# Kernel optimization log

Hardware: AMD Instinct MI355X
Metric: run time of the kernel (lower is better)

## Reference

```python
import jax, jax.numpy as jnp
import numpy as np

B, C, W, H, N = 8, 128, 48, 48, 8192


def setup_inputs() -> dict:
    key = jax.random.key(0)
    ks = jax.random.split(key, 16)
    s = 1.0 / np.sqrt(C)
    inp = {
        "feat0": jax.random.normal(ks[0], (B, C, W, H), jnp.float32),
        "feat1": jax.random.normal(ks[1], (B, C, N), jnp.float32),
        "geo_embed": jax.random.normal(ks[2], (B, W * H, C), jnp.float32),
        # Linear weights stored as [in, out]; biases [out].
        "Wq": jax.random.normal(ks[3], (C, C), jnp.float32) * s,
        "bq": jnp.zeros((C,), jnp.float32),
        "Wk": jax.random.normal(ks[4], (C, C), jnp.float32) * s,
        "bk": jnp.zeros((C,), jnp.float32),
        "Wv": jax.random.normal(ks[5], (C, C), jnp.float32) * s,
        "bv": jnp.zeros((C,), jnp.float32),
        "Wo": jax.random.normal(ks[6], (C, C), jnp.float32) * s,
        "bo": jnp.zeros((C,), jnp.float32),
        "Wg": jax.random.normal(ks[7], (C, C), jnp.float32) * s,
        "bg": jnp.zeros((C,), jnp.float32),
        "Wgate": jax.random.normal(ks[8], (2 * C, 1), jnp.float32) * (1.0 / np.sqrt(2 * C)),
        "bgate": jnp.zeros((1,), jnp.float32),
    }
    return inp


def reference(feat0, feat1, geo_embed, Wq, bq, Wk, bk, Wv, bv, Wo, bo, Wg, bg, Wgate, bgate):
    b, c, w, h = feat0.shape
    # b c w h -> b (w h) c
    q_in = feat0.reshape(b, c, w * h).transpose(0, 2, 1)
    pq = q_in @ Wq + bq  # [b, wh, c]

    geo = geo_embed @ Wg + bg  # [b, wh, c]
    gate = jax.nn.sigmoid(jnp.concatenate([pq, geo], axis=-1) @ Wgate + bgate)  # [b, wh, 1]
    pq = pq + gate * geo

    kv_in = feat1.transpose(0, 2, 1)  # [b, n, c]
    pk = kv_in @ Wk + bk
    pv = kv_in @ Wv + bv

    energy = jnp.einsum('bqc,bnc->bqn', pq, pk)  # [b, wh, n]
    # NOTE: original scales AFTER softmax (non-standard, faithful):
    attention = jax.nn.softmax(energy, axis=-1) / jnp.sqrt(jnp.asarray(c, energy.dtype))
    out = jnp.einsum('bqn,bnc->bqc', attention, pv) @ Wo + bo  # [b, wh, c]
    out = out.transpose(0, 2, 1).reshape(b, c, w, h)

    geo_r = geo.transpose(0, 2, 1).reshape(b, c, w, h)
    out = out * (1.0 + jax.nn.sigmoid(geo_r))
    out = out + feat0
    return out
```

## Files before the change

### kernel.cpp

```cpp
#include <hip/hip_runtime.h>

#define B_ 8
#define C_ 128
#define WH_ 2304
#define N_ 8192

typedef unsigned short u16;
typedef float f32x4 __attribute__((ext_vector_type(4)));
typedef short s16x8 __attribute__((ext_vector_type(8)));
typedef short s16x4 __attribute__((ext_vector_type(4)));
typedef unsigned int u32x2 __attribute__((ext_vector_type(2)));

typedef const unsigned int __attribute__((address_space(1))) ga_u32;
typedef unsigned int __attribute__((address_space(3))) lds_u32;

#define LOG2E 1.4426950408889634f
#define MOFF  64.0f

#define MFMA16K16(a,b,c) __builtin_amdgcn_mfma_f32_16x16x16bf16_1k(a,b,c,0,0,0)

__device__ __forceinline__ float bf2f(u16 u){
    union { unsigned int i; float f; } x; x.i = ((unsigned int)u) << 16; return x.f;
}
__device__ __forceinline__ u16 f2bf(float f){
    union { float f; unsigned int i; } x; x.f = f;
    unsigned int r = x.i + 0x7fffu + ((x.i >> 16) & 1u);
    return (u16)(r >> 16);
}
__device__ __forceinline__ int swz(int row, int col){
    return row*128 + ((((col >> 3) ^ (row & 15)) << 3) | (col & 7));
}
__device__ __forceinline__ f32x4 fzero(){ f32x4 z = {0.f, 0.f, 0.f, 0.f}; return z; }
__device__ __forceinline__ f32x4 mfma16(s16x8 a, s16x8 b, f32x4 c){
    return __builtin_amdgcn_mfma_f32_16x16x32_bf16(a, b, c, 0, 0, 0);
}
__device__ __forceinline__ void gld16(const void* g, void* l){
    __builtin_amdgcn_global_load_lds((ga_u32*)g, (lds_u32*)l, 16, 0, 0);
}
__device__ __forceinline__ s16x8 ldsf(const u16* p){ return *(const s16x8*)p; }
__device__ __forceinline__ s16x4 ldsf4(const u16* p){ return *(const s16x4*)p; }
__device__ __forceinline__ s16x8 cvt8(const float* p){
    s16x8 r;
    #pragma unroll
    for (int j = 0; j < 8; j++) r[j] = (short)f2bf(p[j]);
    return r;
}

__global__ __launch_bounds__(256) void k_prep(
    const float* __restrict__ Wq, const float* __restrict__ Wk,
    const float* __restrict__ Wv, const float* __restrict__ Wo,
    const float* __restrict__ Wg, u16* __restrict__ Wt)
{
    const int gid = blockIdx.x*256 + threadIdx.x;
    const int mi = gid >> 14, e = gid & 16383;
    const int o = e >> 7, i = e & 127;
    const float* src = (mi==0)?Wq:(mi==1)?Wk:(mi==2)?Wv:(mi==3)?Wo:Wg;
    Wt[mi*16384 + o*128 + i] = f2bf(src[i*128 + o]);
}

__device__ __forceinline__ void proj_kv_body(
    char* smem, int blk,
    const float* __restrict__ feat1,
    const float* __restrict__ bk, const float* __restrict__ bv,
    const u16* __restrict__ Wt,
    u16* __restrict__ Kb, u16* __restrict__ Vb)
{
    u16* Wks = (u16*)smem;
    u16* Wvs = (u16*)(smem + 32768);
    u16* Af  = (u16*)(smem + 65536);
    const int t = threadIdx.x;
    const int b = blk >> 5;
    const int n0 = (blk & 31) * 256;
    for (int idx = t; idx < 2048; idx += 256){
        int o = idx >> 4, i0 = (idx & 15) << 3;
        *(s16x8*)&Wks[o*128 + (((i0 >> 3) ^ (o & 15)) << 3)] = *(const s16x8*)&Wt[16384 + o*128 + i0];
        *(s16x8*)&Wvs[o*128 + (((i0 >> 3) ^ (o & 15)) << 3)] = *(const s16x8*)&Wt[32768 + o*128 + i0];
    }
    for (int idx = t; idx < 256*128; idx += 256){
        int nl = idx & 255, c = idx >> 8;
        Af[swz(nl, c)] = f2bf(feat1[((size_t)b*C_ + c)*N_ + n0 + nl]);
    }
    __syncthreads();
    const int lane = t & 63, w = t >> 6, qq = lane >> 4, m = lane & 15;
    s16x8 aA[4][4];
    #pragma unroll
    for (int rt = 0; rt < 4; rt++){
        const int ar = w*64 + rt*16 + m;
        #pragma unroll
        for (int kt = 0; kt < 4; kt++)
            aA[rt][kt] = ldsf(&Af[ar*128 + (((kt*4 + qq) ^ (ar & 15)) << 3)]);
    }
    f32x4 acc[4][8];
    #pragma unroll
    for (int rt = 0; rt < 4; rt++){
        #pragma unroll
        for (int ct = 0; ct < 8; ct++) acc[rt][ct] = fzero();
    }
    #pragma unroll
    for (int kt = 0; kt < 4; kt++){
        #pragma unroll
        for (int ct = 0; ct < 8; ct++){
            const int bn = ct*16 + m;
            const s16x8 bf = ldsf(&Wks[bn*128 + (((kt*4 + qq) ^ (bn & 15)) << 3)]);
            #pragma unroll
            for (int rt = 0; rt < 4; rt++) acc[rt][ct] = mfma16(aA[rt][kt], bf, acc[rt][ct]);
        }
    }
    __syncthreads();
    u16* Ko = (u16*)(smem + 65536);
    #pragma unroll
    for (int ct = 0; ct < 8; ct++){
        const int col = ct*16 + m;
        const float bkv = bk[col];
        #pragma unroll
        for (int rt = 0; rt < 4; rt++){
            #pragma unroll
            for (int i = 0; i < 4; i++)
                Ko[swz(w*64 + rt*16 + qq*4 + i, col)] = f2bf(acc[rt][ct][i] + bkv);
        }
    }
    #pragma unroll
    for (int j = 0; j < 16; j++){
        const int chunk = j*64 + lane;
        const int row = w*64 + (chunk >> 4);
        const int cb = chunk & 15;
        s16x8 v = ldsf(&Ko[row*128 + ((cb ^ (row & 15)) << 3)]);
        *(s16x8*)&Kb[((size_t)b*N_ + n0 + row)*C_ + cb*8] = v;
    }
    #pragma unroll
    for (int rt = 0; rt < 4; rt++){
        #pragma unroll
        for (int ct = 0; ct < 8; ct++) acc[rt][ct] = fzero();
    }
    #pragma unroll
    for (int kt = 0; kt < 4; kt++){
        #pragma unroll
        for (int ct = 0; ct < 8; ct++){
            const int bn = ct*16 + m;
            const s16x8 bf = ldsf(&Wvs[bn*128 + (((kt*4 + qq) ^ (bn & 15)) << 3)]);
            #pragma unroll
            for (int rt = 0; rt < 4; rt++) acc[rt][ct] = mfma16(aA[rt][kt], bf, acc[rt][ct]);
        }
    }
    __syncthreads();
    u16* Tv = (u16*)(smem + 65536);
    #pragma unroll
    for (int ct = 0; ct < 8; ct++){
        const int col = ct*16 + m;
        const float bvv = bv[col];
        #pragma unroll
        for (int rt = 0; rt < 4; rt++){
            #pragma unroll
            for (int i = 0; i < 4; i++)
                Tv[col*258 + w*64 + rt*16 + qq*4 + i] = f2bf(acc[rt][ct][i] + bvv);
        }
    }
    __syncthreads();
    for (int idx = t; idx < 128*256; idx += 256){
        int c = idx >> 8, nl = idx & 255;
        Vb[((size_t)b*C_ + c)*N_ + n0 + nl] = Tv[c*258 + nl];
    }
}

__device__ __forceinline__ void proj_qg_body(
    char* smem, int blk,
    const float* __restrict__ feat0, const float* __restrict__ geo,
    const float* __restrict__ bq, const float* __restrict__ bg,
    const float* __restrict__ Wgate, const float* __restrict__ bgate,
    const u16* __restrict__ Wt,
    u16* __restrict__ Qb, u16* __restrict__ Gb)
{
    u16* Wqs = (u16*)smem;
    u16* Wgs = (u16*)(smem + 32768);
    u16* Aq  = (u16*)(smem + 65536);
    const int t = threadIdx.x;
    const int b = blk / 18;
    const int r0 = (blk % 18) * 128;
    for (int idx = t; idx < 2048; idx += 256){
        int o = idx >> 4, i0 = (idx & 15) << 3;
        *(s16x8*)&Wqs[o*128 + (((i0 >> 3) ^ (o & 15)) << 3)] = *(const s16x8*)&Wt[o*128 + i0];
        *(s16x8*)&Wgs[o*128 + (((i0 >> 3) ^ (o & 15)) << 3)] = *(const s16x8*)&Wt[65536 + o*128 + i0];
    }
    for (int idx = t; idx < 128*128; idx += 256){
        int r = idx & 127, c = idx >> 7;
        Aq[swz(r, c)] = f2bf(feat0[((size_t)b*C_ + c)*WH_ + r0 + r]);
    }
    __syncthreads();
    const int lane = t & 63, w = t >> 6, qq = lane >> 4, m = lane & 15;
    s16x8 aQ[2][4], aG[2][4];
    #pragma unroll
    for (int rt = 0; rt < 2; rt++){
        const int ar = w*32 + rt*16 + m;
        #pragma unroll
        for (int kt = 0; kt < 4; kt++){
            aQ[rt][kt] = ldsf(&Aq[ar*128 + (((kt*4 + qq) ^ (ar & 15)) << 3)]);
            aG[rt][kt] = cvt8(&geo[((size_t)b*WH_ + r0 + ar)*C_ + kt*32 + qq*8]);
        }
    }
    f32x4 accq[2][8], accg[2][8];
    #pragma unroll
    for (int rt = 0; rt < 2; rt++){
        #pragma unroll
        for (int ct = 0; ct < 8; ct++){ accq[rt][ct] = fzero(); accg[rt][ct] = fzero(); }
    }
    #pragma unroll
    for (int kt = 0; kt < 4; kt++){
        #pragma unroll
        for (int ct = 0; ct < 8; ct++){
            const int bn = ct*16 + m;
            const s16x8 b1 = ldsf(&Wqs[bn*128 + (((kt*4 + qq) ^ (bn & 15)) << 3)]);
            const s16x8 b2 = ldsf(&Wgs[bn*128 + (((kt*4 + qq) ^ (bn & 15)) << 3)]);
            #pragma unroll
            for (int rt = 0; rt < 2; rt++){
                accq[rt][ct] = mfma16(aQ[rt][kt], b1, accq[rt][ct]);
                accg[rt][ct] = mfma16(aG[rt][kt], b2, accg[rt][ct]);
            }
        }
    }
    float bqv[8], bgv[8], w1v[8], w2v[8];
    #pragma unroll
    for (int ct = 0; ct < 8; ct++){
        int col = ct*16 + m;
        bqv[ct] = bq[col]; bgv[ct] = bg[col];
        w1v[ct] = Wgate[col]; w2v[ct] = Wgate[C_ + col];
    }
    const float bg0 = bgate[0];
    float gate[2][4];
    #pragma unroll
    for (int rt = 0; rt < 2; rt++){
        #pragma unroll
        for (int i = 0; i < 4; i++){
            float p = 0.f;
            #pragma unroll
            for (int ct = 0; ct < 8; ct++)
                p += (accq[rt][ct][i] + bqv[ct]) * w1v[ct] + (accg[rt][ct][i] + bgv[ct]) * w2v[ct];
            #pragma unroll
            for (int off = 1; off < 16; off <<= 1) p += __shfl_xor(p, off, 64);
            gate[rt][i] = 1.f / (1.f + __expf(-(p + bg0)));
        }
    }
    __syncthreads();
    u16* St = Aq;
    #pragma unroll
    for (int ct = 0; ct < 8; ct++){
        #pragma unroll
        for (int rt = 0; rt < 2; rt++){
            #pragma unroll
            for (int i = 0; i < 4; i++){
                const float ge = accg[rt][ct][i] + bgv[ct];
                const float pq = accq[rt][ct][i] + bqv[ct] + gate[rt][i] * ge;
                St[swz(w*32 + rt*16 + qq*4 + i, ct*16 + m)] = f2bf(pq * LOG2E);
            }
        }
    }
    #pragma unroll
    for (int j = 0; j < 8; j++){
        const int chunk = j*64 + lane;
        const int row = w*32 + (chunk >> 4);
        const int cb = chunk & 15;
        s16x8 v = ldsf(&St[row*128 + ((cb ^ (row & 15)) << 3)]);
        *(s16x8*)&Qb[((size_t)b*WH_ + r0 + row)*C_ + cb*8] = v;
    }
    #pragma unroll
    for (int ct = 0; ct < 8; ct++){
        #pragma unroll
        for (int rt = 0; rt < 2; rt++){
            #pragma unroll
            for (int i = 0; i < 4; i++)
                St[swz(w*32 + rt*16 + qq*4 + i, ct*16 + m)] = f2bf(accg[rt][ct][i] + bgv[ct]);
        }
    }
    #pragma unroll
    for (int j = 0; j < 8; j++){
        const int chunk = j*64 + lane;
        const int row = w*32 + (chunk >> 4);
        const int cb = chunk & 15;
        s16x8 v = ldsf(&St[row*128 + ((cb ^ (row & 15)) << 3)]);
        *(s16x8*)&Gb[((size_t)b*WH_ + r0 + row)*C_ + cb*8] = v;
    }
}

__global__ __launch_bounds__(256) void k_proj(
    const float* __restrict__ feat1,
    const float* __restrict__ bk, const float* __restrict__ bv,
    const float* __restrict__ feat0, const float* __restrict__ geo,
    const float* __restrict__ bq, const float* __restrict__ bg,
    const float* __restrict__ Wgate, const float* __restrict__ bgate,
    const u16* __restrict__ Wt,
    u16* __restrict__ Kb, u16* __restrict__ Vb,
    u16* __restrict__ Qb, u16* __restrict__ Gb)
{
    __shared__ __attribute__((aligned(16))) char smem[65536 + 66048];
    if (blockIdx.x < 256)
        proj_kv_body(smem, blockIdx.x, feat1, bk, bv, Wt, Kb, Vb);
    else
        proj_qg_body(smem, blockIdx.x - 256, feat0, geo, bq, bg, Wgate, bgate, Wt, Qb, Gb);
}

__global__ __launch_bounds__(1024, 4) void k_flash(
    const u16* __restrict__ Qb, const u16* __restrict__ Kb, const u16* __restrict__ Vb,
    u16* __restrict__ Opart, float* __restrict__ Lp)
{
    __shared__ __attribute__((aligned(16))) u16 KP0[128*128];
    __shared__ __attribute__((aligned(16))) u16 KP1[128*128];
    __shared__ __attribute__((aligned(16))) u16 Vt0[128*128];
    __shared__ __attribute__((aligned(16))) u16 Vt1[128*128];
    const int t = threadIdx.x;
    const int lane = t & 63, w = t >> 6;
    const int q = lane >> 4, m = lane & 15;
    const int b = blockIdx.x & 7;
    const int s = blockIdx.x >> 3;

    f32x4 o[8];
    float lr;
    s16x8 qf[4];

    auto issue = [&](int k){
        const int u = s*18 + k;
        const int n0 = (u & 63) * 128;
        u16* KPd = (k & 1) ? KP1 : KP0;
        u16* Vtd = (k & 1) ? Vt1 : Vt0;
        #pragma unroll
        for (int j = 0; j < 2; j++){
            const int r = w*8 + j*4 + q;
            gld16(Kb + ((size_t)b*N_ + n0 + r)*C_ + ((m ^ (r & 15)) << 3), &KPd[(w*8 + j*4)*128]);
            gld16(Vb + ((size_t)b*C_ + r)*N_ + n0 + ((m ^ (r & 15)) << 3), &Vtd[(w*8 + j*4)*128]);
        }
    };
    auto load_q = [&](int qb){
        const size_t qrow0 = (size_t)b*WH_ + qb*256;
        #pragma unroll
        for (int kt = 0; kt < 4; kt++)
            qf[kt] = *(const s16x8*)&Qb[(qrow0 + w*16 + m)*C_ + kt*32 + q*8];
    };
    auto zero_acc = [&](){
        #pragma unroll
        for (int ct = 0; ct < 8; ct++) o[ct] = fzero();
        lr = 0.f;
    };
    auto flush = [&](int qb){
        const int sf = (qb * 64) / 18;
        const size_t pbase = ((size_t)(b*9 + qb)*5 + (s - sf)) * 256;
        #pragma unroll
        for (int ct = 0; ct < 8; ct++){
            u32x2 pk;
            pk.x = (unsigned int)f2bf(o[ct][0]) | ((unsigned int)f2bf(o[ct][1]) << 16);
            pk.y = (unsigned int)f2bf(o[ct][2]) | ((unsigned int)f2bf(o[ct][3]) << 16);
            *(u32x2*)&Opart[(pbase + w*16 + m)*128 + ct*16 + q*4] = pk;
        }
        float l0 = lr;
        l0 += __shfl_xor(l0, 16, 64); l0 += __shfl_xor(l0, 32, 64);
        if (q == 0) Lp[pbase + w*16 + m] = l0;
    };

    issue(0);
    int cur_qb = (s*18) >> 6;
    load_q(cur_qb);
    zero_acc();

    for (int k = 0; k < 18; k++){
        __syncthreads();
        if (k < 17) issue(k + 1);
        const u16* KPc = (k & 1) ? KP1 : KP0;
        const u16* Vtc = (k & 1) ? Vt1 : Vt0;

        #pragma unroll
        for (int h = 0; h < 2; h++){
            s16x4 pexp[4];
            #pragma unroll
            for (int n2 = 0; n2 < 4; n2++){
                const int nt = h*4 + n2;
                f32x4 s0 = fzero();
                const int bn = nt*16 + m;
                #pragma unroll
                for (int kt = 0; kt < 4; kt++){
                    s16x8 kf = ldsf(&KPc[bn*128 + (((kt*4 + q) ^ (bn & 15)) << 3)]);
                    s0 = mfma16(kf, qf[kt], s0);
                }
                #pragma unroll
                for (int i = 0; i < 4; i++){
                    float e0 = exp2f(s0[i] - MOFF);
                    lr += e0;
                    pexp[n2][i] = (short)f2bf(e0);
                }
            }
            #pragma unroll
            for (int ct = 0; ct < 8; ct++){
                const int cc = ct*16 + m;
                #pragma unroll
                for (int n2 = 0; n2 < 4; n2++){
                    const int g = h*4 + n2;
                    s16x4 vf = ldsf4(&Vtc[cc*128 + ((((g*2 + (q >> 1)) ^ (cc & 15)) << 3) | ((q & 1) * 4))]);
                    o[ct] = MFMA16K16(vf, pexp[n2], o[ct]);
                }
            }
        }
        const int nqb = (k < 17) ? ((s*18 + k + 1) >> 6) : -1;
        if (nqb != cur_qb){
            flush(cur_qb);
            if (nqb >= 0){ load_q(nqb); zero_acc(); cur_qb = nqb; }
        }
    }
}

__global__ __launch_bounds__(256) void k_out(
    const u16* __restrict__ Opart, const float* __restrict__ Lp,
    const float* __restrict__ bo, const u16* __restrict__ Wt,
    const u16* __restrict__ Gb, const float* __restrict__ feat0,
    float* __restrict__ outp)
{
    __shared__ __attribute__((aligned(16))) u16 AO[128*128];
    __shared__ u16 Tr[128*130];
    const int t = threadIdx.x;
    const int bqt = blockIdx.x;
    const int qt2 = bqt >> 1, half = bqt & 1;
    const int b = qt2 / 9, qb = qt2 % 9;
    const int gr0 = qb*256 + half*128;
    const u16* WoT = Wt + 49152;
    const float rsC = 0.088388347648318447f;
    const int sf = (qb*64) / 18;
    const int sl = (qb*64 + 63) / 18;
    const int cnt = sl - sf + 1;
    for (int idx = t; idx < 128*16; idx += 256){
        int r = idx >> 4, cb = idx & 15;
        float num[8];
        #pragma unroll
        for (int j = 0; j < 8; j++) num[j] = 0.f;
        float den = 0.f;
        for (int ss = 0; ss < cnt; ss++){
            const size_t base = ((size_t)qt2*5 + ss)*256 + half*128 + r;
            s16x8 v = *(const s16x8*)&Opart[base*128 + cb*8];
            #pragma unroll
            for (int j = 0; j < 8; j++) num[j] += bf2f((u16)v[j]);
            den += Lp[base];
        }
        const float sc = rsC / den;
        s16x8 o8;
        #pragma unroll
        for (int j = 0; j < 8; j++) o8[j] = (short)f2bf(num[j] * sc);
        *(s16x8*)&AO[r*128 + ((cb ^ (r & 15)) << 3)] = o8;
    }
    __syncthreads();
    const int lane = t & 63, w = t >> 6;
    const int q = lane >> 4, m = lane & 15;
    const int rw = w * 32;
    f32x4 acc[2][8];
    #pragma unroll
    for (int rt = 0; rt < 2; rt++){
        #pragma unroll
        for (int ct = 0; ct < 8; ct++) acc[rt][ct] = fzero();
    }
    #pragma unroll
    for (int kt = 0; kt < 4; kt++){
        s16x8 a0, a1;
        { const int ar = rw + m;      a0 = ldsf(&AO[ar*128 + (((kt*4 + q) ^ (ar & 15)) << 3)]); }
        { const int ar = rw + 16 + m; a1 = ldsf(&AO[ar*128 + (((kt*4 + q) ^ (ar & 15)) << 3)]); }
        #pragma unroll
        for (int ct = 0; ct < 8; ct++){
            const s16x8 bb = *(const s16x8*)&WoT[(ct*16 + m)*128 + kt*32 + q*8];
            acc[0][ct] = mfma16(a0, bb, acc[0][ct]);
            acc[1][ct] = mfma16(a1, bb, acc[1][ct]);
        }
    }
    #pragma unroll
    for (int ct = 0; ct < 8; ct++){
        const int col = ct*16 + m;
        const float bov = bo[col];
        #pragma unroll
        for (int rt = 0; rt < 2; rt++){
            #pragma unroll
            for (int i = 0; i < 4; i++){
                const int rl = rw + rt*16 + q*4 + i;
                const float gv = bf2f(Gb[((size_t)b*WH_ + gr0 + rl)*C_ + col]);
                const float sg = 1.f / (1.f + __expf(-gv));
                Tr[rl*130 + col] = f2bf((acc[rt][ct][i] + bov) * (1.f + sg));
            }
        }
    }
    __syncthreads();
    for (int idx = t; idx < 128*128; idx += 256){
        int c = idx >> 7, wh = idx & 127;
        float v = bf2f(Tr[wh*130 + c]) + feat0[(size_t)(b*C_ + c)*WH_ + gr0 + wh];
        outp[(size_t)(b*C_ + c)*WH_ + gr0 + wh] = v;
    }
}

extern "C" void kernel_launch(void* const* d_in, const int* in_sizes, int n_in,
                              void* d_out, int out_size, void* d_ws, size_t ws_size,
                              hipStream_t stream)
{
    (void)in_sizes; (void)n_in; (void)out_size; (void)ws_size;
    const float* feat0 = (const float*)d_in[0];
    const float* feat1 = (const float*)d_in[1];
    const float* geo   = (const float*)d_in[2];
    const float* Wq = (const float*)d_in[3];  const float* bq = (const float*)d_in[4];
    const float* Wk = (const float*)d_in[5];  const float* bk = (const float*)d_in[6];
    const float* Wv = (const float*)d_in[7];  const float* bv = (const float*)d_in[8];
    const float* Wo = (const float*)d_in[9];  const float* bo = (const float*)d_in[10];
    const float* Wg = (const float*)d_in[11]; const float* bg = (const float*)d_in[12];
    const float* Wgate = (const float*)d_in[13]; const float* bgate = (const float*)d_in[14];
    float* outp = (float*)d_out;
    char* ws = (char*)d_ws;
    size_t off = 0;
    auto alloc = [&](size_t bytes) -> void* {
        void* p = (void*)(ws + off);
        off += (bytes + 255) & ~(size_t)255;
        return p;
    };
    u16* Qb = (u16*)alloc((size_t)B_*WH_*C_*2);
    u16* Gb = (u16*)alloc((size_t)B_*WH_*C_*2);
    u16* Kb = (u16*)alloc((size_t)B_*N_*C_*2);
    u16* Vb = (u16*)alloc((size_t)B_*N_*C_*2);
    u16* Opart = (u16*)alloc((size_t)72*5*256*128*2);
    float* Lp  = (float*)alloc((size_t)72*5*256*4);
    u16* Wt = (u16*)alloc((size_t)5*16384*2);

    k_prep <<<dim3(320), dim3(256), 0, stream>>>(Wq, Wk, Wv, Wo, Wg, Wt);
    k_proj <<<dim3(400), dim3(256), 0, stream>>>(feat1, bk, bv, feat0, geo, bq, bg,
                                                 Wgate, bgate, Wt, Kb, Vb, Qb, Gb);
    k_flash<<<dim3(256), dim3(1024), 0, stream>>>(Qb, Kb, Vb, Opart, Lp);
    k_out  <<<dim3(144), dim3(256), 0, stream>>>(Opart, Lp, bo, Wt, Gb, feat0, outp);
}
```

Baseline: 297.6 us.

## Use K=32 MFMA for PV via key permutation and slim projection kernel

The flash kernel permutes key rows during the LDS load so that two 16x16x16 MFMAs per V-tile can be merged into one 16x16x32 bf16 MFMA. The -MOFF softmax offset moves into the MFMA accumulator init, which removes one subtract per score. The projection kernel now runs 512 threads per block with half the rows per wave and reads weights straight from global memory instead of staging them in LDS. Input loads are vectorized, which cuts shared memory use and aims to raise occupancy. The trade-off is more global/L2 weight traffic and a permutation that must exactly match the P-fragment layout.

```diff
diff --git a/kernel.cpp b/kernel.cpp
--- a/kernel.cpp
+++ b/kernel.cpp
@@ -17,8 +17,6 @@
 #define LOG2E 1.4426950408889634f
 #define MOFF  64.0f
 
-#define MFMA16K16(a,b,c) __builtin_amdgcn_mfma_f32_16x16x16bf16_1k(a,b,c,0,0,0)
-
 __device__ __forceinline__ float bf2f(u16 u){
     union { unsigned int i; float f; } x; x.i = ((unsigned int)u) << 16; return x.f;
 }
@@ -31,6 +29,7 @@
     return row*128 + ((((col >> 3) ^ (row & 15)) << 3) | (col & 7));
 }
 __device__ __forceinline__ f32x4 fzero(){ f32x4 z = {0.f, 0.f, 0.f, 0.f}; return z; }
+__device__ __forceinline__ f32x4 fmoff(){ f32x4 z = {-MOFF, -MOFF, -MOFF, -MOFF}; return z; }
 __device__ __forceinline__ f32x4 mfma16(s16x8 a, s16x8 b, f32x4 c){
     return __builtin_amdgcn_mfma_f32_16x16x32_bf16(a, b, c, 0, 0, 0);
 }
@@ -38,7 +37,6 @@
     __builtin_amdgcn_global_load_lds((ga_u32*)g, (lds_u32*)l, 16, 0, 0);
 }
 __device__ __forceinline__ s16x8 ldsf(const u16* p){ return *(const s16x8*)p; }
-__device__ __forceinline__ s16x4 ldsf4(const u16* p){ return *(const s16x4*)p; }
 __device__ __forceinline__ s16x8 cvt8(const float* p){
     s16x8 r;
     #pragma unroll
@@ -65,34 +63,31 @@
     const u16* __restrict__ Wt,
     u16* __restrict__ Kb, u16* __restrict__ Vb)
 {
-    u16* Wks = (u16*)smem;
-    u16* Wvs = (u16*)(smem + 32768);
-    u16* Af  = (u16*)(smem + 65536);
+    u16* Af = (u16*)smem;
     const int t = threadIdx.x;
     const int b = blk >> 5;
     const int n0 = (blk & 31) * 256;
-    for (int idx = t; idx < 2048; idx += 256){
-        int o = idx >> 4, i0 = (idx & 15) << 3;
-        *(s16x8*)&Wks[o*128 + (((i0 >> 3) ^ (o & 15)) << 3)] = *(const s16x8*)&Wt[16384 + o*128 + i0];
-        *(s16x8*)&Wvs[o*128 + (((i0 >> 3) ^ (o & 15)) << 3)] = *(const s16x8*)&Wt[32768 + o*128 + i0];
-    }
-    for (int idx = t; idx < 256*128; idx += 256){
-        int nl = idx & 255, c = idx >> 8;
-        Af[swz(nl, c)] = f2bf(feat1[((size_t)b*C_ + c)*N_ + n0 + nl]);
+    for (int idx = t; idx < 8192; idx += 512){
+        const int nl = (idx & 63) << 2, c = idx >> 6;
+        const f32x4 v = *(const f32x4*)&feat1[((size_t)b*C_ + c)*N_ + n0 + nl];
+        Af[swz(nl+0, c)] = f2bf(v[0]); Af[swz(nl+1, c)] = f2bf(v[1]);
+        Af[swz(nl+2, c)] = f2bf(v[2]); Af[swz(nl+3, c)] = f2bf(v[3]);
     }
     __syncthreads();
     const int lane = t & 63, w = t >> 6, qq = lane >> 4, m = lane & 15;
-    s16x8 aA[4][4];
-    #pragma unroll
-    for (int rt = 0; rt < 4; rt++){
-        const int ar = w*64 + rt*16 + m;
+    s16x8 aA[2][4];
+    #pragma unroll
+    for (int rt = 0; rt < 2; rt++){
+        const int ar = w*32 + rt*16 + m;
         #pragma unroll
         for (int kt = 0; kt < 4; kt++)
             aA[rt][kt] = ldsf(&Af[ar*128 + (((kt*4 + qq) ^ (ar & 15)) << 3)]);
     }
-    f32x4 acc[4][8];
-    #pragma unroll
-    for (int rt = 0; rt < 4; rt++){
+    const u16* WkT = Wt + 16384;
+    const u16* WvT = Wt + 32768;
+    f32x4 acc[2][8];
+    #pragma unroll
+    for (int rt = 0; rt < 2; rt++){
         #pragma unroll
         for (int ct = 0; ct < 8; ct++) acc[rt][ct] = fzero();
     }
@@ -101,34 +96,33 @@
         #pragma unroll
         for (int ct = 0; ct < 8; ct++){
             const int bn = ct*16 + m;
-            const s16x8 bf = ldsf(&Wks[bn*128 + (((kt*4 + qq) ^ (bn & 15)) << 3)]);
-            #pragma unroll
-            for (int rt = 0; rt < 4; rt++) acc[rt][ct] = mfma16(aA[rt][kt], bf, acc[rt][ct]);
-        }
-    }
-    __syncthreads();
-    u16* Ko = (u16*)(smem + 65536);
+            const s16x8 bf = *(const s16x8*)&WkT[bn*128 + kt*32 + qq*8];
+            acc[0][ct] = mfma16(aA[0][kt], bf, acc[0][ct]);
+            acc[1][ct] = mfma16(aA[1][kt], bf, acc[1][ct]);
+        }
+    }
+    u16* Ko = (u16*)smem;
     #pragma unroll
     for (int ct = 0; ct < 8; ct++){
         const int col = ct*16 + m;
         const float bkv = bk[col];
         #pragma unroll
-        for (int rt = 0; rt < 4; rt++){
+        for (int rt = 0; rt < 2; rt++){
             #pragma unroll
             for (int i = 0; i < 4; i++)
-                Ko[swz(w*64 + rt*16 + qq*4 + i, col)] = f2bf(acc[rt][ct][i] + bkv);
-        }
-    }
-    #pragma unroll
-    for (int j = 0; j < 16; j++){
+                Ko[swz(w*32 + rt*16 + qq*4 + i, col)] = f2bf(acc[rt][ct][i] + bkv);
+        }
+    }
+    #pragma unroll
+    for (int j = 0; j < 8; j++){
         const int chunk = j*64 + lane;
-        const int row = w*64 + (chunk >> 4);
+        const int row = w*32 + (chunk >> 4);
         const int cb = chunk & 15;
         s16x8 v = ldsf(&Ko[row*128 + ((cb ^ (row & 15)) << 3)]);
         *(s16x8*)&Kb[((size_t)b*N_ + n0 + row)*C_ + cb*8] = v;
     }
     #pragma unroll
-    for (int rt = 0; rt < 4; rt++){
+    for (int rt = 0; rt < 2; rt++){
         #pragma unroll
         for (int ct = 0; ct < 8; ct++) acc[rt][ct] = fzero();
     }
@@ -137,28 +131,29 @@
         #pragma unroll
         for (int ct = 0; ct < 8; ct++){
             const int bn = ct*16 + m;
-            const s16x8 bf = ldsf(&Wvs[bn*128 + (((kt*4 + qq) ^ (bn & 15)) << 3)]);
-            #pragma unroll
-            for (int rt = 0; rt < 4; rt++) acc[rt][ct] = mfma16(aA[rt][kt], bf, acc[rt][ct]);
-        }
-    }
-    __syncthreads();
-    u16* Tv = (u16*)(smem + 65536);
+            const s16x8 bf = *(const s16x8*)&WvT[bn*128 + kt*32 + qq*8];
+            acc[0][ct] = mfma16(aA[0][kt], bf, acc[0][ct]);
+            acc[1][ct] = mfma16(aA[1][kt], bf, acc[1][ct]);
+        }
+    }
+    __syncthreads();
+    u16* Tv = (u16*)smem;
     #pragma unroll
     for (int ct = 0; ct < 8; ct++){
         const int col = ct*16 + m;
         const float bvv = bv[col];
         #pragma unroll
-        for (int rt = 0; rt < 4; rt++){
+        for (int rt = 0; rt < 2; rt++){
             #pragma unroll
             for (int i = 0; i < 4; i++)
-                Tv[col*258 + w*64 + rt*16 + qq*4 + i] = f2bf(acc[rt][ct][i] + bvv);
-        }
-    }
-    __syncthreads();
-    for (int idx = t; idx < 128*256; idx += 256){
-        int c = idx >> 8, nl = idx & 255;
-        Vb[((size_t)b*C_ + c)*N_ + n0 + nl] = Tv[c*258 + nl];
+                Tv[col*258 + w*32 + rt*16 + qq*4 + i] = f2bf(acc[rt][ct][i] + bvv);
+        }
+    }
+    __syncthreads();
+    for (int idx = t; idx < 16384; idx += 512){
+        const int c = idx >> 7, nl = (idx & 127) << 1;
+        const unsigned int v = *(const unsigned int*)&Tv[c*258 + nl];
+        *(unsigned int*)&Vb[((size_t)b*C_ + c)*N_ + n0 + nl] = v;
     }
 }
 
@@ -170,51 +165,37 @@
     const u16* __restrict__ Wt,
     u16* __restrict__ Qb, u16* __restrict__ Gb)
 {
-    u16* Wqs = (u16*)smem;
-    u16* Wgs = (u16*)(smem + 32768);
-    u16* Aq  = (u16*)(smem + 65536);
+    u16* Aq = (u16*)smem;
     const int t = threadIdx.x;
     const int b = blk / 18;
     const int r0 = (blk % 18) * 128;
-    for (int idx = t; idx < 2048; idx += 256){
-        int o = idx >> 4, i0 = (idx & 15) << 3;
-        *(s16x8*)&Wqs[o*128 + (((i0 >> 3) ^ (o & 15)) << 3)] = *(const s16x8*)&Wt[o*128 + i0];
-        *(s16x8*)&Wgs[o*128 + (((i0 >> 3) ^ (o & 15)) << 3)] = *(const s16x8*)&Wt[65536 + o*128 + i0];
-    }
-    for (int idx = t; idx < 128*128; idx += 256){
-        int r = idx & 127, c = idx >> 7;
-        Aq[swz(r, c)] = f2bf(feat0[((size_t)b*C_ + c)*WH_ + r0 + r]);
+    for (int idx = t; idx < 4096; idx += 512){
+        const int r = (idx & 31) << 2, c = idx >> 5;
+        const f32x4 v = *(const f32x4*)&feat0[((size_t)b*C_ + c)*WH_ + r0 + r];
+        Aq[swz(r+0, c)] = f2bf(v[0]); Aq[swz(r+1, c)] = f2bf(v[1]);
+        Aq[swz(r+2, c)] = f2bf(v[2]); Aq[swz(r+3, c)] = f2bf(v[3]);
     }
     __syncthreads();
     const int lane = t & 63, w = t >> 6, qq = lane >> 4, m = lane & 15;
-    s16x8 aQ[2][4], aG[2][4];
-    #pragma unroll
-    for (int rt = 0; rt < 2; rt++){
-        const int ar = w*32 + rt*16 + m;
-        #pragma unroll
-        for (int kt = 0; kt < 4; kt++){
-            aQ[rt][kt] = ldsf(&Aq[ar*128 + (((kt*4 + qq) ^ (ar & 15)) << 3)]);
-            aG[rt][kt] = cvt8(&geo[((size_t)b*WH_ + r0 + ar)*C_ + kt*32 + qq*8]);
-        }
-    }
-    f32x4 accq[2][8], accg[2][8];
-    #pragma unroll
-    for (int rt = 0; rt < 2; rt++){
-        #pragma unroll
-        for (int ct = 0; ct < 8; ct++){ accq[rt][ct] = fzero(); accg[rt][ct] = fzero(); }
-    }
+    const int ar = w*16 + m;
+    s16x8 aQ[4], aG[4];
+    #pragma unroll
+    for (int kt = 0; kt < 4; kt++){
+        aQ[kt] = ldsf(&Aq[ar*128 + (((kt*4 + qq) ^ (ar & 15)) << 3)]);
+        aG[kt] = cvt8(&geo[((size_t)b*WH_ + r0 + ar)*C_ + kt*32 + qq*8]);
+    }
+    f32x4 accq[8], accg[8];
+    #pragma unroll
+    for (int ct = 0; ct < 8; ct++){ accq[ct] = fzero(); accg[ct] = fzero(); }
     #pragma unroll
     for (int kt = 0; kt < 4; kt++){
         #pragma unroll
         for (int ct = 0; ct < 8; ct++){
             const int bn = ct*16 + m;
-            const s16x8 b1 = ldsf(&Wqs[bn*128 + (((kt*4 + qq) ^ (bn & 15)) << 3)]);
-            const s16x8 b2 = ldsf(&Wgs[bn*128 + (((kt*4 + qq) ^ (bn & 15)) << 3)]);
-            #pragma unroll
-            for (int rt = 0; rt < 2; rt++){
-                accq[rt][ct] = mfma16(aQ[rt][kt], b1, accq[rt][ct]);
-                accg[rt][ct] = mfma16(aG[rt][kt], b2, accg[rt][ct]);
-            }
+            const s16x8 b1 = *(const s16x8*)&Wt[bn*128 + kt*32 + qq*8];
+            const s16x8 b2 = *(const s16x8*)&Wt[65536 + bn*128 + kt*32 + qq*8];
+            accq[ct] = mfma16(aQ[kt], b1, accq[ct]);
+            accg[ct] = mfma16(aG[kt], b2, accg[ct]);
         }
     }
     float bqv[8], bgv[8], w1v[8], w2v[8];
@@ -225,38 +206,31 @@
         w1v[ct] = Wgate[col]; w2v[ct] = Wgate[C_ + col];
     }
     const float bg0 = bgate[0];
-    float gate[2][4];
-    #pragma unroll
-    for (int rt = 0; rt < 2; rt++){
+    float gate[4];
+    #pragma unroll
+    for (int i = 0; i < 4; i++){
+        float p = 0.f;
+        #pragma unroll
+        for (int ct = 0; ct < 8; ct++)
+            p += (accq[ct][i] + bqv[ct]) * w1v[ct] + (accg[ct][i] + bgv[ct]) * w2v[ct];
+        #pragma unroll
+        for (int off = 1; off < 16; off <<= 1) p += __shfl_xor(p, off, 64);
+        gate[i] = 1.f / (1.f + __expf(-(p + bg0)));
+    }
+    u16* St = Aq;
+    #pragma unroll
+    for (int ct = 0; ct < 8; ct++){
         #pragma unroll
         for (int i = 0; i < 4; i++){
-            float p = 0.f;
-            #pragma unroll
-            for (int ct = 0; ct < 8; ct++)
-                p += (accq[rt][ct][i] + bqv[ct]) * w1v[ct] + (accg[rt][ct][i] + bgv[ct]) * w2v[ct];
-            #pragma unroll
-            for (int off = 1; off < 16; off <<= 1) p += __shfl_xor(p, off, 64);
-            gate[rt][i] = 1.f / (1.f + __expf(-(p + bg0)));
-        }
-    }
-    __syncthreads();
-    u16* St = Aq;
-    #pragma unroll
-    for (int ct = 0; ct < 8; ct++){
-        #pragma unroll
-        for (int rt = 0; rt < 2; rt++){
-            #pragma unroll
-            for (int i = 0; i < 4; i++){
-                const float ge = accg[rt][ct][i] + bgv[ct];
-                const float pq = accq[rt][ct][i] + bqv[ct] + gate[rt][i] * ge;
-                St[swz(w*32 + rt*16 + qq*4 + i, ct*16 + m)] = f2bf(pq * LOG2E);
-            }
-        }
-    }
-    #pragma unroll
-    for (int j = 0; j < 8; j++){
+            const float ge = accg[ct][i] + bgv[ct];
+            const float pq = accq[ct][i] + bqv[ct] + gate[i] * ge;
+            St[swz(w*16 + qq*4 + i, ct*16 + m)] = f2bf(pq * LOG2E);
+        }
+    }
+    #pragma unroll
+    for (int j = 0; j < 4; j++){
         const int chunk = j*64 + lane;
-        const int row = w*32 + (chunk >> 4);
+        const int row = w*16 + (chunk >> 4);
         const int cb = chunk & 15;
         s16x8 v = ldsf(&St[row*128 + ((cb ^ (row & 15)) << 3)]);
         *(s16x8*)&Qb[((size_t)b*WH_ + r0 + row)*C_ + cb*8] = v;
@@ -264,23 +238,20 @@
     #pragma unroll
     for (int ct = 0; ct < 8; ct++){
         #pragma unroll
-        for (int rt = 0; rt < 2; rt++){
-            #pragma unroll
-            for (int i = 0; i < 4; i++)
-                St[swz(w*32 + rt*16 + qq*4 + i, ct*16 + m)] = f2bf(accg[rt][ct][i] + bgv[ct]);
-        }
-    }
-    #pragma unroll
-    for (int j = 0; j < 8; j++){
+        for (int i = 0; i < 4; i++)
+            St[swz(w*16 + qq*4 + i, ct*16 + m)] = f2bf(accg[ct][i] + bgv[ct]);
+    }
+    #pragma unroll
+    for (int j = 0; j < 4; j++){
         const int chunk = j*64 + lane;
-        const int row = w*32 + (chunk >> 4);
+        const int row = w*16 + (chunk >> 4);
         const int cb = chunk & 15;
         s16x8 v = ldsf(&St[row*128 + ((cb ^ (row & 15)) << 3)]);
         *(s16x8*)&Gb[((size_t)b*WH_ + r0 + row)*C_ + cb*8] = v;
     }
 }
 
-__global__ __launch_bounds__(256) void k_proj(
+__global__ __launch_bounds__(512, 4) void k_proj(
     const float* __restrict__ feat1,
     const float* __restrict__ bk, const float* __restrict__ bv,
     const float* __restrict__ feat0, const float* __restrict__ geo,
@@ -290,7 +261,7 @@
     u16* __restrict__ Kb, u16* __restrict__ Vb,
     u16* __restrict__ Qb, u16* __restrict__ Gb)
 {
-    __shared__ __attribute__((aligned(16))) char smem[65536 + 66048];
+    __shared__ __attribute__((aligned(16))) char smem[66048];
     if (blockIdx.x < 256)
         proj_kv_body(smem, blockIdx.x, feat1, bk, bv, Wt, Kb, Vb);
     else
@@ -323,7 +294,8 @@
         #pragma unroll
         for (int j = 0; j < 2; j++){
             const int r = w*8 + j*4 + q;
-            gld16(Kb + ((size_t)b*N_ + n0 + r)*C_ + ((m ^ (r & 15)) << 3), &KPd[(w*8 + j*4)*128]);
+            const int pr = (r & 96) | ((r & 12) << 1) | ((r & 16) >> 2) | (r & 3);
+            gld16(Kb + ((size_t)b*N_ + n0 + pr)*C_ + ((m ^ (r & 15)) << 3), &KPd[(w*8 + j*4)*128]);
             gld16(Vb + ((size_t)b*C_ + r)*N_ + n0 + ((m ^ (r & 15)) << 3), &Vtd[(w*8 + j*4)*128]);
         }
     };
@@ -370,7 +342,7 @@
             #pragma unroll
             for (int n2 = 0; n2 < 4; n2++){
                 const int nt = h*4 + n2;
-                f32x4 s0 = fzero();
+                f32x4 s0 = fmoff();
                 const int bn = nt*16 + m;
                 #pragma unroll
                 for (int kt = 0; kt < 4; kt++){
@@ -379,20 +351,21 @@
                 }
                 #pragma unroll
                 for (int i = 0; i < 4; i++){
-                    float e0 = exp2f(s0[i] - MOFF);
+                    float e0 = exp2f(s0[i]);
                     lr += e0;
                     pexp[n2][i] = (short)f2bf(e0);
                 }
             }
+            const s16x8 p80 = __builtin_shufflevector(pexp[0], pexp[1], 0,1,2,3,4,5,6,7);
+            const s16x8 p81 = __builtin_shufflevector(pexp[2], pexp[3], 0,1,2,3,4,5,6,7);
             #pragma unroll
             for (int ct = 0; ct < 8; ct++){
                 const int cc = ct*16 + m;
-                #pragma unroll
-                for (int n2 = 0; n2 < 4; n2++){
-                    const int g = h*4 + n2;
-                    s16x4 vf = ldsf4(&Vtc[cc*128 + ((((g*2 + (q >> 1)) ^ (cc & 15)) << 3) | ((q & 1) * 4))]);
-                    o[ct] = MFMA16K16(vf, pexp[n2], o[ct]);
-                }
+                const int pair0 = h*2;
+                s16x8 vf0 = ldsf(&Vtc[cc*128 + ((((pair0+0)*4 + q) ^ (cc & 15)) << 3)]);
+                s16x8 vf1 = ldsf(&Vtc[cc*128 + ((((pair0+1)*4 + q) ^ (cc & 15)) << 3)]);
+                o[ct] = mfma16(vf0, p80, o[ct]);
+                o[ct] = mfma16(vf1, p81, o[ct]);
             }
         }
         const int nqb = (k < 17) ? ((s*18 + k + 1) >> 6) : -1;
@@ -516,7 +489,7 @@
     u16* Wt = (u16*)alloc((size_t)5*16384*2);
 
     k_prep <<<dim3(320), dim3(256), 0, stream>>>(Wq, Wk, Wv, Wo, Wg, Wt);
-    k_proj <<<dim3(400), dim3(256), 0, stream>>>(feat1, bk, bv, feat0, geo, bq, bg,
+    k_proj <<<dim3(400), dim3(512), 0, stream>>>(feat1, bk, bv, feat0, geo, bq, bg,
                                                  Wgate, bgate, Wt, Kb, Vb, Qb, Gb);
     k_flash<<<dim3(256), dim3(1024), 0, stream>>>(Qb, Kb, Vb, Opart, Lp);
     k_out  <<<dim3(144), dim3(256), 0, stream>>>(Opart, Lp, bo, Wt, Gb, feat0, outp);
```

Result: no change. 303.4 us (+2.0%).

## Use K=32 MFMA for PV via permuted K rows; MFMA row-sum; packed bf16 cvt

Applied to the files above, without the earlier changes.

Permutes K rows at load time so the P fragments produced by the QK MFMA line up with the K=32 bf16 MFMA operand layout. This lets the PV product use half as many 16x16x32 MFMAs with 16-byte V loads, replacing the 16x16x16 ones with 8-byte loads. The softmax denominator is now accumulated with an extra MFMA against a ones vector, which removes the per-element adds and the cross-lane shuffles. The max offset is folded into the accumulator init, and a packed bf16 conversion instruction replaces the manual rounding. The permutation has to match the fragment layout exactly, and the row-sum now uses the bf16-rounded probabilities rather than fp32 values.

```diff
diff --git a/kernel.cpp b/kernel.cpp
--- a/kernel.cpp
+++ b/kernel.cpp
@@ -17,8 +17,6 @@
 #define LOG2E 1.4426950408889634f
 #define MOFF  64.0f
 
-#define MFMA16K16(a,b,c) __builtin_amdgcn_mfma_f32_16x16x16bf16_1k(a,b,c,0,0,0)
-
 __device__ __forceinline__ float bf2f(u16 u){
     union { unsigned int i; float f; } x; x.i = ((unsigned int)u) << 16; return x.f;
 }
@@ -27,10 +25,16 @@
     unsigned int r = x.i + 0x7fffu + ((x.i >> 16) & 1u);
     return (u16)(r >> 16);
 }
+__device__ __forceinline__ unsigned int cvtpk(float a, float b){
+    unsigned int r;
+    asm("v_cvt_pk_bf16_f32 %0, %1, %2" : "=v"(r) : "v"(a), "v"(b));
+    return r;
+}
 __device__ __forceinline__ int swz(int row, int col){
     return row*128 + ((((col >> 3) ^ (row & 15)) << 3) | (col & 7));
 }
 __device__ __forceinline__ f32x4 fzero(){ f32x4 z = {0.f, 0.f, 0.f, 0.f}; return z; }
+__device__ __forceinline__ f32x4 fmoff(){ f32x4 z = {-MOFF, -MOFF, -MOFF, -MOFF}; return z; }
 __device__ __forceinline__ f32x4 mfma16(s16x8 a, s16x8 b, f32x4 c){
     return __builtin_amdgcn_mfma_f32_16x16x32_bf16(a, b, c, 0, 0, 0);
 }
@@ -38,7 +42,6 @@
     __builtin_amdgcn_global_load_lds((ga_u32*)g, (lds_u32*)l, 16, 0, 0);
 }
 __device__ __forceinline__ s16x8 ldsf(const u16* p){ return *(const s16x8*)p; }
-__device__ __forceinline__ s16x4 ldsf4(const u16* p){ return *(const s16x4*)p; }
 __device__ __forceinline__ s16x8 cvt8(const float* p){
     s16x8 r;
     #pragma unroll
@@ -312,8 +315,11 @@
     const int s = blockIdx.x >> 3;
 
     f32x4 o[8];
-    float lr;
+    f32x4 l_acc;
     s16x8 qf[4];
+    s16x8 ones8;
+    #pragma unroll
+    for (int j = 0; j < 8; j++) ones8[j] = (short)0x3F80;
 
     auto issue = [&](int k){
         const int u = s*18 + k;
@@ -323,7 +329,8 @@
         #pragma unroll
         for (int j = 0; j < 2; j++){
             const int r = w*8 + j*4 + q;
-            gld16(Kb + ((size_t)b*N_ + n0 + r)*C_ + ((m ^ (r & 15)) << 3), &KPd[(w*8 + j*4)*128]);
+            const int pr = (r & 96) | ((r & 12) << 1) | ((r & 16) >> 2) | (r & 3);
+            gld16(Kb + ((size_t)b*N_ + n0 + pr)*C_ + ((m ^ (r & 15)) << 3), &KPd[(w*8 + j*4)*128]);
             gld16(Vb + ((size_t)b*C_ + r)*N_ + n0 + ((m ^ (r & 15)) << 3), &Vtd[(w*8 + j*4)*128]);
         }
     };
@@ -336,7 +343,7 @@
     auto zero_acc = [&](){
         #pragma unroll
         for (int ct = 0; ct < 8; ct++) o[ct] = fzero();
-        lr = 0.f;
+        l_acc = fzero();
     };
     auto flush = [&](int qb){
         const int sf = (qb * 64) / 18;
@@ -344,13 +351,11 @@
         #pragma unroll
         for (int ct = 0; ct < 8; ct++){
             u32x2 pk;
-            pk.x = (unsigned int)f2bf(o[ct][0]) | ((unsigned int)f2bf(o[ct][1]) << 16);
-            pk.y = (unsigned int)f2bf(o[ct][2]) | ((unsigned int)f2bf(o[ct][3]) << 16);
+            pk.x = cvtpk(o[ct][0], o[ct][1]);
+            pk.y = cvtpk(o[ct][2], o[ct][3]);
             *(u32x2*)&Opart[(pbase + w*16 + m)*128 + ct*16 + q*4] = pk;
         }
-        float l0 = lr;
-        l0 += __shfl_xor(l0, 16, 64); l0 += __shfl_xor(l0, 32, 64);
-        if (q == 0) Lp[pbase + w*16 + m] = l0;
+        if (q == 0) Lp[pbase + w*16 + m] = l_acc[0];
     };
 
     issue(0);
@@ -370,29 +375,30 @@
             #pragma unroll
             for (int n2 = 0; n2 < 4; n2++){
                 const int nt = h*4 + n2;
-                f32x4 s0 = fzero();
+                f32x4 s0 = fmoff();
                 const int bn = nt*16 + m;
                 #pragma unroll
                 for (int kt = 0; kt < 4; kt++){
                     s16x8 kf = ldsf(&KPc[bn*128 + (((kt*4 + q) ^ (bn & 15)) << 3)]);
                     s0 = mfma16(kf, qf[kt], s0);
                 }
-                #pragma unroll
-                for (int i = 0; i < 4; i++){
-                    float e0 = exp2f(s0[i] - MOFF);
-                    lr += e0;
-                    pexp[n2][i] = (short)f2bf(e0);
-                }
+                union { u32x2 u; s16x4 v; } pp;
+                pp.u.x = cvtpk(exp2f(s0[0]), exp2f(s0[1]));
+                pp.u.y = cvtpk(exp2f(s0[2]), exp2f(s0[3]));
+                pexp[n2] = pp.v;
             }
+            const s16x8 p80 = __builtin_shufflevector(pexp[0], pexp[1], 0,1,2,3,4,5,6,7);
+            const s16x8 p81 = __builtin_shufflevector(pexp[2], pexp[3], 0,1,2,3,4,5,6,7);
+            l_acc = mfma16(ones8, p80, l_acc);
+            l_acc = mfma16(ones8, p81, l_acc);
             #pragma unroll
             for (int ct = 0; ct < 8; ct++){
                 const int cc = ct*16 + m;
-                #pragma unroll
-                for (int n2 = 0; n2 < 4; n2++){
-                    const int g = h*4 + n2;
-                    s16x4 vf = ldsf4(&Vtc[cc*128 + ((((g*2 + (q >> 1)) ^ (cc & 15)) << 3) | ((q & 1) * 4))]);
-                    o[ct] = MFMA16K16(vf, pexp[n2], o[ct]);
-                }
+                const int pair0 = h*2;
+                s16x8 vf0 = ldsf(&Vtc[cc*128 + ((((pair0+0)*4 + q) ^ (cc & 15)) << 3)]);
+                s16x8 vf1 = ldsf(&Vtc[cc*128 + ((((pair0+1)*4 + q) ^ (cc & 15)) << 3)]);
+                o[ct] = mfma16(vf0, p80, o[ct]);
+                o[ct] = mfma16(vf1, p81, o[ct]);
             }
         }
         const int nqb = (k < 17) ? ((s*18 + k + 1) >> 6) : -1;
```

Result: faster. 280.1 us (-5.9%).
